# Kernel tuning notes

Measured on AMD Instinct MI355X. Metric: run time of the kernel, lower is better.

The kernel has to match this reference:

```python
import jax, jax.numpy as jnp
import numpy as np

TEMPERATURE = 0.2


def setup_inputs() -> dict:
    key = jax.random.key(0)
    k1, k2, k3, k4 = jax.random.split(key, 4)
    B, D, K, C = 8192, 128, 10, 10
    x = jax.random.normal(k1, (B, D), dtype=jnp.float32)
    x_aug = jax.random.normal(k2, (B, D), dtype=jnp.float32)
    hard_q = jax.random.randint(k3, (2, B), 0, C, dtype=jnp.int64)
    neg_q = jax.random.randint(k4, (2, B, K), 0, C, dtype=jnp.int64)
    return {"x": x, "x_aug": x_aug, "hard_q": hard_q, "neg_q": neg_q,
            "num_clusters": C}


def reference(x, x_aug, hard_q, neg_q, num_clusters):
    B = x.shape[0]
    N = 2 * B
    # L2-normalize both views and concatenate: out is [2B, D]
    out_1 = x / jnp.linalg.norm(x, axis=1, keepdims=True)
    out_2 = x_aug / jnp.linalg.norm(x_aug, axis=1, keepdims=True)
    out = jnp.concatenate([out_1, out_2], axis=0)

    hq = hard_q.reshape(N)            # [2B] cluster id per sample
    nq = neg_q.reshape(N, -1)         # [2B, K] negative cluster ids per row

    # exp(similarity / T): [2B, 2B]
    sim_matrix = jnp.exp(jnp.matmul(out, out.T) / TEMPERATURE)

    # membership[i, j] = (hard_q[j] in neg_q[i]).
    # Build a small [2B, C] cluster-membership table instead of a [2B,2B,K]
    # broadcast to keep memory low, then gather columns by hq.
    cluster_ids = jnp.arange(num_clusters)                       # [C]
    table = jnp.any(nq[:, :, None] == cluster_ids[None, None, :], axis=1)  # [2B, C]
    member = table[:, hq]                                        # [2B, 2B]

    eye = jnp.eye(N, dtype=bool)
    mask = member & ~eye

    # Original code does masked_select (flatten) then .sum(dim=-1), which
    # reduces over ALL selected entries -> a single scalar denominator.
    denom = jnp.sum(jnp.where(mask, sim_matrix, jnp.float32(0.0)))

    pos = jnp.exp(jnp.sum(out_1 * out_2, axis=-1) / TEMPERATURE)  # [B]
    pos = jnp.concatenate([pos, pos], axis=0)                     # [2B]

    loss = jnp.mean(-jnp.log(pos / denom))
    return loss
```

## Files before the change

### kernel.cpp

```cpp
#include <hip/hip_runtime.h>
#include <hip/hip_bf16.h>

typedef __attribute__((ext_vector_type(8))) __bf16 bf16x8;
typedef __attribute__((ext_vector_type(4))) float f32x4;

#define SCALE 2.68588886f

static __device__ __forceinline__ float fastexp2(float x) {
#if __has_builtin(__builtin_amdgcn_exp2f)
    return __builtin_amdgcn_exp2f(x);
#else
    return exp2f(x);
#endif
}


__global__ __launch_bounds__(256) void normalize_kernel(
    const float* __restrict__ x, const float* __restrict__ xa,
    __bf16* __restrict__ outb, float* __restrict__ pos_parts, int B)
{
    __shared__ float sdot[4];
    int wave = threadIdx.x >> 6;
    int lane = threadIdx.x & 63;
    int row = blockIdx.x * 4 + wave;
    const float2* px = (const float2*)(x  + (size_t)row * 128);
    const float2* pa = (const float2*)(xa + (size_t)row * 128);
    float2 v1 = px[lane];
    float2 v2 = pa[lane];
    float s1 = v1.x * v1.x + v1.y * v1.y;
    float s2 = v2.x * v2.x + v2.y * v2.y;
    float d  = v1.x * v2.x + v1.y * v2.y;
    #pragma unroll
    for (int off = 32; off; off >>= 1) {
        s1 += __shfl_xor(s1, off);
        s2 += __shfl_xor(s2, off);
        d  += __shfl_xor(d,  off);
    }
    float rn1 = rsqrtf(s1) * SCALE;
    float rn2 = rsqrtf(s2) * SCALE;
    __bf16* o1 = outb + (size_t)row * 128;
    __bf16* o2 = outb + (size_t)(B + row) * 128;
    o1[2 * lane]     = (__bf16)(v1.x * rn1);
    o1[2 * lane + 1] = (__bf16)(v1.y * rn1);
    o2[2 * lane]     = (__bf16)(v2.x * rn2);
    o2[2 * lane + 1] = (__bf16)(v2.y * rn2);
    if (lane == 0) sdot[wave] = d * rsqrtf(s1) * rsqrtf(s2);
    __syncthreads();
    if (threadIdx.x == 0)
        pos_parts[blockIdx.x] = sdot[0] + sdot[1] + sdot[2] + sdot[3];
}

__global__ __launch_bounds__(256, 4) void sim_kernel(
    const __bf16* __restrict__ outb, const int* __restrict__ hq,
    const int* __restrict__ nq, float* __restrict__ denom_parts)
{
    int t = blockIdx.x;
    int bi = (int)(128.5f - sqrtf(128.5f * 128.5f - 2.0f * (float)t));
    if (bi < 0) bi = 0;
    if (bi > 127) bi = 127;
    while (128 * (bi + 1) - ((bi + 1) * bi) / 2 <= t) ++bi;
    while (128 * bi - (bi * (bi - 1)) / 2 > t) --bi;
    int bj = bi + (t - (128 * bi - (bi * (bi - 1)) / 2));

    __shared__ __bf16 lA[128 * 64];
    __shared__ __bf16 lB[128 * 64];
    __shared__ unsigned sMU[128];
    __shared__ unsigned sMV[128];
    __shared__ float red[4];

    int tid = threadIdx.x;

    {
        int half = tid >> 7;
        int idx = tid & 127;
        int row = (half ? bj : bi) * 128 + idx;
        const int* p = nq + (size_t)row * 10;
        unsigned b = 0;
        #pragma unroll
        for (int k = 0; k < 10; ++k) b |= 1u << (p[k] & 31);
        unsigned h = (unsigned)hq[row];
        if (half) sMV[idx] = (1u << h) | (b << 10);
        else      sMU[idx] = b | (1u << (10 + h));
    }

    const float4* gA = (const float4*)(outb + (size_t)bi * 128 * 128);
    const float4* gB = (const float4*)(outb + (size_t)bj * 128 * 128);
    float4* sA4 = (float4*)lA;
    float4* sB4 = (float4*)lB;

    int wave = tid >> 6, lane = tid & 63;
    int wr = (wave >> 1) * 64;
    int wc = (wave & 1) * 64;
    int lrow = lane & 15, quad = lane >> 4;

    f32x4 acc[4][4] = {};

    #pragma unroll
    for (int ph = 0; ph < 2; ++ph) {
        if (ph) __syncthreads();
        #pragma unroll
        for (int it = 0; it < 4; ++it) {
            int ci = it * 256 + tid;
            int row = ci >> 3;
            int c = ci & 7;
            int pos = c ^ (row & 7);
            sA4[row * 8 + pos] = gA[row * 16 + ph * 8 + c];
            sB4[row * 8 + pos] = gB[row * 16 + ph * 8 + c];
        }
        __syncthreads();
        #pragma unroll
        for (int kk = 0; kk < 2; ++kk) {
            int chunk = kk * 4 + quad;
            bf16x8 a[4], b[4];
            #pragma unroll
            for (int m = 0; m < 4; ++m) {
                int r = wr + m * 16 + lrow;
                a[m] = *(const bf16x8*)&lA[r * 64 + ((chunk ^ (r & 7)) << 3)];
            }
            #pragma unroll
            for (int n = 0; n < 4; ++n) {
                int r = wc + n * 16 + lrow;
                b[n] = *(const bf16x8*)&lB[r * 64 + ((chunk ^ (r & 7)) << 3)];
            }
            #pragma unroll
            for (int m = 0; m < 4; ++m)
                #pragma unroll
                for (int n = 0; n < 4; ++n)
                    acc[m][n] = __builtin_amdgcn_mfma_f32_16x16x32_bf16(
                        a[m], b[n], acc[m][n], 0, 0, 0);
        }
    }

    unsigned mv[4], mu[4][4];
    #pragma unroll
    for (int n = 0; n < 4; ++n) mv[n] = sMV[wc + n * 16 + lrow];
    #pragma unroll
    for (int m = 0; m < 4; ++m)
        #pragma unroll
        for (int r = 0; r < 4; ++r) mu[m][r] = sMU[wr + m * 16 + quad * 4 + r];

    float ls[4] = {0.0f, 0.0f, 0.0f, 0.0f};
    bool diag = (bi == bj);
    #pragma unroll
    for (int m = 0; m < 4; ++m) {
        #pragma unroll
        for (int n = 0; n < 4; ++n) {
            #pragma unroll
            for (int r = 0; r < 4; ++r) {
                float w = (float)__popc(mu[m][r] & mv[n]);
                if (diag && (wr + m * 16 + quad * 4 + r) == (wc + n * 16 + lrow))
                    w = 0.0f;
                ls[r] += fastexp2(acc[m][n][r]) * w;
            }
        }
    }
    float lsum = (ls[0] + ls[1]) + (ls[2] + ls[3]);
    if (diag) lsum *= 0.5f;

    #pragma unroll
    for (int off = 32; off; off >>= 1) lsum += __shfl_down(lsum, off);
    if (lane == 0) red[wave] = lsum;
    __syncthreads();
    if (tid == 0)
        denom_parts[blockIdx.x] = red[0] + red[1] + red[2] + red[3];
}

__global__ __launch_bounds__(1024) void finalize_kernel(
    const float* __restrict__ denom_parts, const float* __restrict__ pos_parts,
    float* __restrict__ out, float invB, int nd, int np)
{
    __shared__ float sred[32];
    int tid = threadIdx.x;
    float d = 0.0f, p = 0.0f;
    for (int i = tid; i < nd; i += 1024) d += denom_parts[i];
    for (int i = tid; i < np; i += 1024) p += pos_parts[i];
    #pragma unroll
    for (int off = 32; off; off >>= 1) {
        d += __shfl_down(d, off);
        p += __shfl_down(p, off);
    }
    int wv = tid >> 6, ln = tid & 63;
    if (ln == 0) { sred[wv] = d; sred[16 + wv] = p; }
    __syncthreads();
    if (tid == 0) {
        float D = 0.0f, P = 0.0f;
        #pragma unroll
        for (int i = 0; i < 16; ++i) { D += sred[i]; P += sred[16 + i]; }
        out[0] = logf(D) - 5.0f * P * invB;
    }
}

extern "C" void kernel_launch(void* const* d_in, const int* in_sizes, int n_in,
                              void* d_out, int out_size, void* d_ws, size_t ws_size,
                              hipStream_t stream) {
    const float* x  = (const float*)d_in[0];
    const float* xa = (const float*)d_in[1];
    const int* hq   = (const int*)d_in[2];
    const int* nq   = (const int*)d_in[3];
    int B = in_sizes[0] / 128;
    int N = 2 * B;
    int T = N / 128;
    int nblocks = T * (T + 1) / 2;

    char* ws = (char*)d_ws;
    float* denom_parts = (float*)ws;
    float* pos_parts   = (float*)(ws + 33024);
    __bf16* outb       = (__bf16*)(ws + 41216);

    normalize_kernel<<<B / 4, 256, 0, stream>>>(x, xa, outb, pos_parts, B);
    sim_kernel<<<nblocks, 256, 0, stream>>>(outb, hq, nq, denom_parts);
    finalize_kernel<<<1, 1024, 0, stream>>>(denom_parts, pos_parts,
                                            (float*)d_out, 1.0f / (float)B,
                                            nblocks, B / 4);
}
```

Measured before the change: 124.5 us.

## Use direct global-to-LDS loads and split the diagonal epilogue in sim kernel

Tile staging now uses global_load_lds to move bf16 tiles straight into LDS, skipping the trip through VGPRs. The swizzle moves from the LDS write side to the global read side, and the first-phase loads are issued before the mask-table setup so the two overlap. The epilogue is split into separate off-diagonal and diagonal branches, so the common path drops the per-element diagonal compare, and the normalize kernel packs its bf16 pairs into 32-bit stores. The risk is that the per-lane LDS destination for the direct load may not match what the builtin actually writes (it uses an M0 base plus lane offset), and no explicit wait is placed before the barrier.

```diff
diff --git a/kernel.cpp b/kernel.cpp
--- a/kernel.cpp
+++ b/kernel.cpp
@@ -12,6 +12,12 @@
 #else
     return exp2f(x);
 #endif
+}
+
+typedef __attribute__((address_space(1))) const unsigned int gu32_t;
+typedef __attribute__((address_space(3))) unsigned int lu32_t;
+static __device__ __forceinline__ void load16_to_lds(const void* g, void* l) {
+    __builtin_amdgcn_global_load_lds((gu32_t*)g, (lu32_t*)l, 16, 0, 0);
 }
 
 
@@ -38,12 +44,11 @@
     }
     float rn1 = rsqrtf(s1) * SCALE;
     float rn2 = rsqrtf(s2) * SCALE;
-    __bf16* o1 = outb + (size_t)row * 128;
-    __bf16* o2 = outb + (size_t)(B + row) * 128;
-    o1[2 * lane]     = (__bf16)(v1.x * rn1);
-    o1[2 * lane + 1] = (__bf16)(v1.y * rn1);
-    o2[2 * lane]     = (__bf16)(v2.x * rn2);
-    o2[2 * lane + 1] = (__bf16)(v2.y * rn2);
+    union { __bf16 h[2]; unsigned u; } p1, p2;
+    p1.h[0] = (__bf16)(v1.x * rn1); p1.h[1] = (__bf16)(v1.y * rn1);
+    p2.h[0] = (__bf16)(v2.x * rn2); p2.h[1] = (__bf16)(v2.y * rn2);
+    ((unsigned*)(outb + (size_t)row * 128))[lane]       = p1.u;
+    ((unsigned*)(outb + (size_t)(B + row) * 128))[lane] = p2.u;
     if (lane == 0) sdot[wave] = d * rsqrtf(s1) * rsqrtf(s2);
     __syncthreads();
     if (threadIdx.x == 0)
@@ -69,6 +74,19 @@
     __shared__ float red[4];
 
     int tid = threadIdx.x;
+    const float4* gA = (const float4*)(outb + (size_t)bi * 128 * 128);
+    const float4* gB = (const float4*)(outb + (size_t)bj * 128 * 128);
+    float4* sA4 = (float4*)lA;
+    float4* sB4 = (float4*)lB;
+
+    #pragma unroll
+    for (int it = 0; it < 4; ++it) {
+        int ci = it * 256 + tid;
+        int row = ci >> 3;
+        int gc = (ci & 7) ^ (row & 7);
+        load16_to_lds(&gA[row * 16 + gc], &sA4[ci]);
+        load16_to_lds(&gB[row * 16 + gc], &sB4[ci]);
+    }
 
     {
         int half = tid >> 7;
@@ -83,11 +101,6 @@
         else      sMU[idx] = b | (1u << (10 + h));
     }
 
-    const float4* gA = (const float4*)(outb + (size_t)bi * 128 * 128);
-    const float4* gB = (const float4*)(outb + (size_t)bj * 128 * 128);
-    float4* sA4 = (float4*)lA;
-    float4* sB4 = (float4*)lB;
-
     int wave = tid >> 6, lane = tid & 63;
     int wr = (wave >> 1) * 64;
     int wc = (wave & 1) * 64;
@@ -97,15 +110,16 @@
 
     #pragma unroll
     for (int ph = 0; ph < 2; ++ph) {
-        if (ph) __syncthreads();
-        #pragma unroll
-        for (int it = 0; it < 4; ++it) {
-            int ci = it * 256 + tid;
-            int row = ci >> 3;
-            int c = ci & 7;
-            int pos = c ^ (row & 7);
-            sA4[row * 8 + pos] = gA[row * 16 + ph * 8 + c];
-            sB4[row * 8 + pos] = gB[row * 16 + ph * 8 + c];
+        if (ph) {
+            __syncthreads();
+            #pragma unroll
+            for (int it = 0; it < 4; ++it) {
+                int ci = it * 256 + tid;
+                int row = ci >> 3;
+                int gc = (ci & 7) ^ (row & 7);
+                load16_to_lds(&gA[row * 16 + 8 + gc], &sA4[ci]);
+                load16_to_lds(&gB[row * 16 + 8 + gc], &sB4[ci]);
+            }
         }
         __syncthreads();
         #pragma unroll
@@ -140,22 +154,33 @@
         for (int r = 0; r < 4; ++r) mu[m][r] = sMU[wr + m * 16 + quad * 4 + r];
 
     float ls[4] = {0.0f, 0.0f, 0.0f, 0.0f};
-    bool diag = (bi == bj);
-    #pragma unroll
-    for (int m = 0; m < 4; ++m) {
-        #pragma unroll
-        for (int n = 0; n < 4; ++n) {
-            #pragma unroll
-            for (int r = 0; r < 4; ++r) {
-                float w = (float)__popc(mu[m][r] & mv[n]);
-                if (diag && (wr + m * 16 + quad * 4 + r) == (wc + n * 16 + lrow))
-                    w = 0.0f;
-                ls[r] += fastexp2(acc[m][n][r]) * w;
+    float lsum;
+    if (bi != bj) {
+        #pragma unroll
+        for (int m = 0; m < 4; ++m)
+            #pragma unroll
+            for (int n = 0; n < 4; ++n)
+                #pragma unroll
+                for (int r = 0; r < 4; ++r)
+                    ls[r] += fastexp2(acc[m][n][r]) *
+                             (float)__popc(mu[m][r] & mv[n]);
+        lsum = (ls[0] + ls[1]) + (ls[2] + ls[3]);
+    } else {
+        #pragma unroll
+        for (int m = 0; m < 4; ++m) {
+            #pragma unroll
+            for (int n = 0; n < 4; ++n) {
+                #pragma unroll
+                for (int r = 0; r < 4; ++r) {
+                    float w = (float)__popc(mu[m][r] & mv[n]);
+                    if ((wr + m * 16 + quad * 4 + r) == (wc + n * 16 + lrow))
+                        w = 0.0f;
+                    ls[r] += fastexp2(acc[m][n][r]) * w;
+                }
             }
         }
-    }
-    float lsum = (ls[0] + ls[1]) + (ls[2] + ls[3]);
-    if (diag) lsum *= 0.5f;
+        lsum = ((ls[0] + ls[1]) + (ls[2] + ls[3])) * 0.5f;
+    }
 
     #pragma unroll
     for (int off = 32; off; off >>= 1) lsum += __shfl_down(lsum, off);
```

After: 198.6 us. 59.6% more time.
